# Kernel tuning notes

Measured on AMD Instinct MI355X. Metric: run time of the kernel, lower is better.

## Reference

```python
import jax, jax.numpy as jnp
import numpy as np

VOCAB = 50257
EMBED_DIM = 768
NUM_TUNE = 1024


def setup_inputs() -> dict:
    key = jax.random.key(0)
    k_ids, k_tune, k_base, k_train = jax.random.split(key, 4)
    input_ids = jax.random.randint(k_ids, (8, 4096), 0, VOCAB, dtype=jnp.int64)
    tune_ids = jnp.sort(jax.random.randint(k_tune, (NUM_TUNE,), 0, VOCAB, dtype=jnp.int64))
    base_weight = jax.random.normal(k_base, (VOCAB, EMBED_DIM), dtype=jnp.float32)
    # In the torch module train_weight is initialized from base rows; independent init is fine for a numeric baseline.
    train_weight = jax.random.normal(k_train, (NUM_TUNE, EMBED_DIM), dtype=jnp.float32)
    return {"input_ids": input_ids, "tune_ids": tune_ids,
            "base_weight": base_weight, "train_weight": train_weight}


def reference(input_ids, tune_ids, base_weight, train_weight):
    # Precompute id -> train-row mapping (replaces the torch.isin + python-loop dict lookup).
    id2row = jnp.full((VOCAB,), -1, dtype=jnp.int32)
    id2row = id2row.at[tune_ids].set(jnp.arange(NUM_TUNE, dtype=jnp.int32))
    out = base_weight[input_ids]                      # [B, S, D] gather
    rows = id2row[input_ids]                          # [B, S] train-row index or -1
    mask = rows >= 0
    override = train_weight[jnp.maximum(rows, 0)]     # [B, S, D]
    return jnp.where(mask[..., None], override, out)
```

## Files before the change

kernel.cpp:

```cpp
#include <hip/hip_runtime.h>


#define EMBED_DIM 768
#define EMBED_DIM4 (EMBED_DIM / 4)
#define WAVES_PER_BLOCK 4
#define BLOCK_THREADS (WAVES_PER_BLOCK * 64)

__global__ __launch_bounds__(BLOCK_THREADS) void split_embedding_kernel(
    const int* __restrict__ input_ids,
    const int* __restrict__ tune_ids,
    const float* __restrict__ base_weight,
    const float* __restrict__ train_weight,
    float* __restrict__ out,
    int num_tokens, int num_tune)
{
    const int wave = threadIdx.x >> 6;
    const int lane = threadIdx.x & 63;
    const int token = blockIdx.x * WAVES_PER_BLOCK + wave;
    if (token >= num_tokens) return;

    const int tok = input_ids[token];

    int lo = 0, hi = num_tune;
    while (lo < hi) {
        const int mid = (lo + hi) >> 1;
        if (tune_ids[mid] <= tok) lo = mid + 1;
        else                      hi = mid;
    }
    const int cand = lo - 1;

    const float4* src;
    if (cand >= 0 && tune_ids[cand] == tok) {
        src = (const float4*)(train_weight + (size_t)cand * EMBED_DIM);
    } else {
        src = (const float4*)(base_weight + (size_t)tok * EMBED_DIM);
    }
    float4* dst = (float4*)(out + (size_t)token * EMBED_DIM);

    #pragma unroll
    for (int i = 0; i < EMBED_DIM4 / 64; ++i) {
        const int c = lane + i * 64;
        dst[c] = src[c];
    }
}

extern "C" void kernel_launch(void* const* d_in, const int* in_sizes, int n_in,
                              void* d_out, int out_size, void* d_ws, size_t ws_size,
                              hipStream_t stream) {
    const int*   input_ids    = (const int*)d_in[0];
    const int*   tune_ids     = (const int*)d_in[1];
    const float* base_weight  = (const float*)d_in[2];
    const float* train_weight = (const float*)d_in[3];
    float*       out          = (float*)d_out;

    const int num_tokens = in_sizes[0];
    const int num_tune   = in_sizes[1];

    const int grid = (num_tokens + WAVES_PER_BLOCK - 1) / WAVES_PER_BLOCK;
    split_embedding_kernel<<<grid, BLOCK_THREADS, 0, stream>>>(
        input_ids, tune_ids, base_weight, train_weight, out, num_tokens, num_tune);
}
```

Measured before the change: 245.3 us.

## Split lookup into LDS binary-search pass and batched nontemporal row-copy pass

```diff
diff --git a/kernel.cpp b/kernel.cpp
--- a/kernel.cpp
+++ b/kernel.cpp
@@ -1,46 +1,89 @@
 #include <hip/hip_runtime.h>
 
 
-#define EMBED_DIM 768
-#define EMBED_DIM4 (EMBED_DIM / 4)
+#define EMBED_DIM   768
 #define WAVES_PER_BLOCK 4
-#define BLOCK_THREADS (WAVES_PER_BLOCK * 64)
+#define TOK_PER_WAVE 4
+#define TOK_PER_BLOCK (WAVES_PER_BLOCK * TOK_PER_WAVE)
+#define MISS_FLAG 0x40000000
 
-__global__ __launch_bounds__(BLOCK_THREADS) void split_embedding_kernel(
-    const int* __restrict__ input_ids,
-    const int* __restrict__ tune_ids,
-    const float* __restrict__ base_weight,
-    const float* __restrict__ train_weight,
-    float* __restrict__ out,
-    int num_tokens, int num_tune)
+typedef __attribute__((ext_vector_type(4))) float f4;
+
+__global__ __launch_bounds__(256) void build_rows_kernel(
+    const int* __restrict__ input_ids, const int* __restrict__ tune_ids,
+    int* __restrict__ enc, int num_tokens, int num_tune)
+{
+    __shared__ int lds_tune[2048];
+    const bool use_lds = (num_tune <= 2048);
+    if (use_lds) {
+        for (int i = threadIdx.x; i < num_tune; i += 256)
+            lds_tune[i] = tune_ids[i];
+        __syncthreads();
+    }
+    const int t = blockIdx.x * 256 + threadIdx.x;
+    if (t >= num_tokens) return;
+
+    const int tok = input_ids[t];
+    const int* tab = use_lds ? lds_tune : tune_ids;
+    int lo = 0, hi = num_tune;
+    while (lo < hi) {
+        const int mid = (lo + hi) >> 1;
+        if (tab[mid] <= tok) lo = mid + 1;
+        else                 hi = mid;
+    }
+    const int cand = lo - 1;
+    const bool hit = (cand >= 0) && (tab[cand] == tok);
+    enc[t] = hit ? cand : (MISS_FLAG | tok);
+}
+
+__device__ __forceinline__ const f4* decode(int e, const float* base, const float* train) {
+    return (e & MISS_FLAG)
+        ? (const f4*)(base  + (size_t)(e & (MISS_FLAG - 1)) * EMBED_DIM)
+        : (const f4*)(train + (size_t)e * EMBED_DIM);
+}
+
+__global__ __launch_bounds__(256) void copy_rows_kernel(
+    const int* __restrict__ enc,
+    const float* __restrict__ base_weight, const float* __restrict__ train_weight,
+    float* __restrict__ out, int num_tokens)
 {
     const int wave = threadIdx.x >> 6;
     const int lane = threadIdx.x & 63;
-    const int token = blockIdx.x * WAVES_PER_BLOCK + wave;
-    if (token >= num_tokens) return;
+    const int tb   = (blockIdx.x * WAVES_PER_BLOCK + wave) * TOK_PER_WAVE;
+    if (tb >= num_tokens) return;
 
-    const int tok = input_ids[token];
+    if (tb + TOK_PER_WAVE <= num_tokens) {
+        const int4 e4 = *(const int4*)(enc + tb);
+        const f4* s0 = decode(e4.x, base_weight, train_weight);
+        const f4* s1 = decode(e4.y, base_weight, train_weight);
+        const f4* s2 = decode(e4.z, base_weight, train_weight);
+        const f4* s3 = decode(e4.w, base_weight, train_weight);
 
-    int lo = 0, hi = num_tune;
-    while (lo < hi) {
-        const int mid = (lo + hi) >> 1;
-        if (tune_ids[mid] <= tok) lo = mid + 1;
-        else                      hi = mid;
-    }
-    const int cand = lo - 1;
+        f4 v[12];
+        #pragma unroll
+        for (int c = 0; c < 3; ++c) v[0 * 3 + c] = s0[lane + c * 64];
+        #pragma unroll
+        for (int c = 0; c < 3; ++c) v[1 * 3 + c] = s1[lane + c * 64];
+        #pragma unroll
+        for (int c = 0; c < 3; ++c) v[2 * 3 + c] = s2[lane + c * 64];
+        #pragma unroll
+        for (int c = 0; c < 3; ++c) v[3 * 3 + c] = s3[lane + c * 64];
 
-    const float4* src;
-    if (cand >= 0 && tune_ids[cand] == tok) {
-        src = (const float4*)(train_weight + (size_t)cand * EMBED_DIM);
+        #pragma unroll
+        for (int t = 0; t < 4; ++t) {
+            f4* dst = (f4*)(out + (size_t)(tb + t) * EMBED_DIM);
+            #pragma unroll
+            for (int c = 0; c < 3; ++c)
+                __builtin_nontemporal_store(v[t * 3 + c], dst + lane + c * 64);
+        }
     } else {
-        src = (const float4*)(base_weight + (size_t)tok * EMBED_DIM);
-    }
-    float4* dst = (float4*)(out + (size_t)token * EMBED_DIM);
-
-    #pragma unroll
-    for (int i = 0; i < EMBED_DIM4 / 64; ++i) {
-        const int c = lane + i * 64;
-        dst[c] = src[c];
+        for (int t = tb; t < num_tokens; ++t) {
+            const f4* src = decode(enc[t], base_weight, train_weight);
+            f4* dst = (f4*)(out + (size_t)t * EMBED_DIM);
+            #pragma unroll
+            for (int c = 0; c < 3; ++c)
+                __builtin_nontemporal_store(src[lane + c * 64], dst + lane + c * 64);
+        }
     }
 }
 
@@ -52,11 +95,16 @@
     const float* base_weight  = (const float*)d_in[2];
     const float* train_weight = (const float*)d_in[3];
     float*       out          = (float*)d_out;
+    int*         enc          = (int*)d_ws;
 
     const int num_tokens = in_sizes[0];
     const int num_tune   = in_sizes[1];
 
-    const int grid = (num_tokens + WAVES_PER_BLOCK - 1) / WAVES_PER_BLOCK;
-    split_embedding_kernel<<<grid, BLOCK_THREADS, 0, stream>>>(
-        input_ids, tune_ids, base_weight, train_weight, out, num_tokens, num_tune);
+    const int gridA = (num_tokens + 255) / 256;
+    build_rows_kernel<<<gridA, 256, 0, stream>>>(input_ids, tune_ids, enc,
+                                                 num_tokens, num_tune);
+
+    const int gridB = (num_tokens + TOK_PER_BLOCK - 1) / TOK_PER_BLOCK;
+    copy_rows_kernel<<<gridB, 256, 0, stream>>>(enc, base_weight, train_weight,
+                                                out, num_tokens);
 }
```

Result: no change. 245.9 us (+0.3%).
